# Performance work log

Measured on AMD Instinct MI355X. Metric: run time of the kernel, lower is better.

The kernel has to match this reference:

```python
import jax, jax.numpy as jnp
import numpy as np

RC = 4.6  # cutoff radius (Angstrom), from init_kwargs
FACTOR = 7.199822675975224  # constants.half_Hartree * constants.Bohr (eV*A)


def exp_cutoff(d, rc):
    # smooth exponential (bump) cutoff: exp(1 - 1/(1-(d/rc)^2)) for d<rc, else 0
    x = d / rc
    inside = x < 1.0
    xs = jnp.where(inside, x, 0.5)  # safe value to avoid nan in masked branch
    f = jnp.exp(1.0 - 1.0 / (1.0 - xs * xs))
    return jnp.where(inside, f, 0.0)


def setup_inputs() -> dict:
    key = jax.random.key(0)
    k1, k2 = jax.random.split(key)
    B, N = 64, 512
    # atoms in a 40 A box -> realistic long-range distances
    coord = jax.random.uniform(k1, (B, N, 3), dtype=jnp.float32) * 40.0
    charges = jax.random.normal(k2, (B, N), dtype=jnp.float32) * 0.3
    mask = jnp.ones((B, N), dtype=bool)  # all atoms valid (no padding)
    return {"coord": coord, "charges": charges, "mask": mask}


def reference(coord, charges, mask):
    # coul_simple: e = factor * sum_ij (1 - fc(d_ij)) * q_i * q_j / d_ij, per molecule
    B, N, _ = coord.shape
    pair_mask = mask[:, :, None] & mask[:, None, :]
    eye = jnp.eye(N, dtype=bool)[None]
    valid = pair_mask & ~eye  # mask self-pairs and padding (mask_ij_)
    disp = coord[:, :, None, :] - coord[:, None, :, :]          # [B,N,N,3]
    d2 = jnp.sum(disp * disp, axis=-1)                          # [B,N,N]
    d = jnp.sqrt(jnp.where(valid, d2, 1.0))                     # safe sqrt on diag
    fc = 1.0 - exp_cutoff(d, RC)
    qq = charges[:, :, None] * charges[:, None, :]              # q_i * q_j
    e_ij = jnp.where(valid, fc * qq / d, 0.0)
    return FACTOR * jnp.sum(e_ij, axis=(1, 2))                  # mol_sum -> [B]
```

## Files before the change

kernel.cpp:

```cpp
#include <hip/hip_runtime.h>

#define N_ATOMS 512
#define SPLITS  16
#define IPB     32
#define BLOCK   256
#define JSTR    8
#define FACTOR  7.199822675975224f

__global__ __launch_bounds__(BLOCK) void coul_pair_kernel(
    const float* __restrict__ coord,
    const float* __restrict__ charges,
    float* __restrict__ partials)
{
    const int b = blockIdx.x >> 4;
    const int s = blockIdx.x & 15;

    __shared__ float4 atom[2 * N_ATOMS];

    const float* c = coord   + (size_t)b * N_ATOMS * 3;
    const float* q = charges + (size_t)b * N_ATOMS;
    for (int k = threadIdx.x; k < N_ATOMS; k += BLOCK) {
        float4 a = make_float4(c[3 * k], c[3 * k + 1], c[3 * k + 2], q[k]);
        atom[k]           = a;
        atom[k + N_ATOMS] = a;
    }
    __syncthreads();

    const int t  = threadIdx.x;
    const int j0 = t & (JSTR - 1);
    const int i  = s * IPB + (t >> 3);

    const float4 ai = atom[i];
    const float inv_rc2 = 1.0f / (4.6f * 4.6f);
    const float4* __restrict__ base = &atom[i + 1 + j0];

    float acc = 0.0f;
    #pragma unroll 8
    for (int k = 0; k < 31; ++k) {
        const float4 aj = base[JSTR * k];
        float dx = ai.x - aj.x, dy = ai.y - aj.y, dz = ai.z - aj.z;
        float d2 = dx * dx + dy * dy + dz * dz;
        float term = ai.w * aj.w * rsqrtf(d2);
        float x2 = d2 * inv_rc2;
        if (x2 < 1.0f)
            term *= (1.0f - __expf(1.0f - 1.0f / (1.0f - x2)));
        acc += term;
    }
    {
        const float4 aj = base[JSTR * 31];
        float dx = ai.x - aj.x, dy = ai.y - aj.y, dz = ai.z - aj.z;
        float d2 = dx * dx + dy * dy + dz * dz;
        float term = ai.w * aj.w * rsqrtf(d2);
        float x2 = d2 * inv_rc2;
        if (x2 < 1.0f)
            term *= (1.0f - __expf(1.0f - 1.0f / (1.0f - x2)));
        acc += (j0 == JSTR - 1) ? 0.5f * term : term;
    }

    #pragma unroll
    for (int off = 32; off > 0; off >>= 1)
        acc += __shfl_down(acc, off, 64);

    __shared__ float wsum[BLOCK / 64];
    if ((t & 63) == 0) wsum[t >> 6] = acc;
    __syncthreads();
    if (t == 0)
        partials[blockIdx.x] = wsum[0] + wsum[1] + wsum[2] + wsum[3];
}

__global__ void coul_reduce_kernel(const float* __restrict__ partials,
                                   float* __restrict__ out, int B)
{
    const int b = threadIdx.x;
    if (b < B) {
        float sum = 0.0f;
        #pragma unroll
        for (int s = 0; s < SPLITS; ++s) sum += partials[b * SPLITS + s];
        out[b] = 2.0f * FACTOR * sum;
    }
}

extern "C" void kernel_launch(void* const* d_in, const int* in_sizes, int n_in,
                              void* d_out, int out_size, void* d_ws, size_t ws_size,
                              hipStream_t stream) {
    const float* coord   = (const float*)d_in[0];
    const float* charges = (const float*)d_in[1];
    float* out      = (float*)d_out;
    float* partials = (float*)d_ws;

    const int B = in_sizes[1] / N_ATOMS;

    coul_pair_kernel<<<B * SPLITS, BLOCK, 0, stream>>>(coord, charges, partials);
    coul_reduce_kernel<<<1, 64, 0, stream>>>(partials, out, B);
}
```

Baseline: 64.44 us.

## Fuse partial reduction into pair kernel via cooperative grid sync

Replaces the separate reduction kernel with a cooperative launch: after writing per-block partials, all blocks perform a grid-wide sync and block 0 sums the partials with float4 loads and writes the outputs. The aim is to remove the second kernel launch and its launch gap. In exchange, every block must wait at the grid barrier, and the cooperative launch needs all 1024 blocks to be co-resident. The cutoff test is also rewritten to compare d2 against rc^2 directly, and the batch size is derived with a heuristic based on byte sizes.

```diff
diff --git a/kernel.cpp b/kernel.cpp
--- a/kernel.cpp
+++ b/kernel.cpp
@@ -1,4 +1,7 @@
 #include <hip/hip_runtime.h>
+#include <hip/hip_cooperative_groups.h>
+
+namespace cg = cooperative_groups;
 
 #define N_ATOMS 512
 #define SPLITS  16
@@ -6,11 +9,13 @@
 #define BLOCK   256
 #define JSTR    8
 #define FACTOR  7.199822675975224f
+#define RC2     (4.6f * 4.6f)
 
-__global__ __launch_bounds__(BLOCK) void coul_pair_kernel(
+__global__ __launch_bounds__(BLOCK) void coul_fused_kernel(
     const float* __restrict__ coord,
     const float* __restrict__ charges,
-    float* __restrict__ partials)
+    float* __restrict__ partials,
+    float* __restrict__ out)
 {
     const int b = blockIdx.x >> 4;
     const int s = blockIdx.x & 15;
@@ -31,7 +36,7 @@
     const int i  = s * IPB + (t >> 3);
 
     const float4 ai = atom[i];
-    const float inv_rc2 = 1.0f / (4.6f * 4.6f);
+    const float inv_rc2 = 1.0f / RC2;
     const float4* __restrict__ base = &atom[i + 1 + j0];
 
     float acc = 0.0f;
@@ -41,9 +46,8 @@
         float dx = ai.x - aj.x, dy = ai.y - aj.y, dz = ai.z - aj.z;
         float d2 = dx * dx + dy * dy + dz * dz;
         float term = ai.w * aj.w * rsqrtf(d2);
-        float x2 = d2 * inv_rc2;
-        if (x2 < 1.0f)
-            term *= (1.0f - __expf(1.0f - 1.0f / (1.0f - x2)));
+        if (d2 < RC2)
+            term *= (1.0f - __expf(1.0f - 1.0f / (1.0f - d2 * inv_rc2)));
         acc += term;
     }
     {
@@ -51,9 +55,8 @@
         float dx = ai.x - aj.x, dy = ai.y - aj.y, dz = ai.z - aj.z;
         float d2 = dx * dx + dy * dy + dz * dz;
         float term = ai.w * aj.w * rsqrtf(d2);
-        float x2 = d2 * inv_rc2;
-        if (x2 < 1.0f)
-            term *= (1.0f - __expf(1.0f - 1.0f / (1.0f - x2)));
+        if (d2 < RC2)
+            term *= (1.0f - __expf(1.0f - 1.0f / (1.0f - d2 * inv_rc2)));
         acc += (j0 == JSTR - 1) ? 0.5f * term : term;
     }
 
@@ -66,17 +69,22 @@
     __syncthreads();
     if (t == 0)
         partials[blockIdx.x] = wsum[0] + wsum[1] + wsum[2] + wsum[3];
-}
 
-__global__ void coul_reduce_kernel(const float* __restrict__ partials,
-                                   float* __restrict__ out, int B)
-{
-    const int b = threadIdx.x;
-    if (b < B) {
-        float sum = 0.0f;
-        #pragma unroll
-        for (int s = 0; s < SPLITS; ++s) sum += partials[b * SPLITS + s];
-        out[b] = 2.0f * FACTOR * sum;
+    __threadfence();
+    cg::this_grid().sync();
+
+    if (blockIdx.x == 0) {
+        const int B = (int)(gridDim.x >> 4);
+        if (t < B) {
+            const float4* p4 =
+                reinterpret_cast<const float4*>(partials) + t * (SPLITS / 4);
+            float4 v0 = p4[0], v1 = p4[1], v2 = p4[2], v3 = p4[3];
+            float sum = (v0.x + v0.y + v0.z + v0.w)
+                      + (v1.x + v1.y + v1.z + v1.w)
+                      + (v2.x + v2.y + v2.z + v2.w)
+                      + (v3.x + v3.y + v3.z + v3.w);
+            out[t] = 2.0f * FACTOR * sum;
+        }
     }
 }
 
@@ -88,8 +96,13 @@
     float* out      = (float*)d_out;
     float* partials = (float*)d_ws;
 
-    const int B = in_sizes[1] / N_ATOMS;
+    const int B = (n_in > 2 && in_sizes[1] != in_sizes[2])
+                      ? in_sizes[1] / (N_ATOMS * 4)
+                      : in_sizes[1] / N_ATOMS;
 
-    coul_pair_kernel<<<B * SPLITS, BLOCK, 0, stream>>>(coord, charges, partials);
-    coul_reduce_kernel<<<1, 64, 0, stream>>>(partials, out, B);
+    void* args[] = { (void*)&coord, (void*)&charges,
+                     (void*)&partials, (void*)&out };
+    hipLaunchCooperativeKernel((const void*)coul_fused_kernel,
+                               dim3(B * SPLITS), dim3(BLOCK),
+                               args, 0, stream);
 }
```

Measured after the change: 170.1 us. 2.64x slower.
